# Kernel tuning notes

Measured on AMD Instinct MI355X. Metric: run time of the kernel, lower is better.

Reference implementation:

```python
import jax, jax.numpy as jnp
import numpy as np

L, H, P_LOC = 32768, 512, 256  # seq len, in/out dim, local state dim (conj_sym: P//2)
DT_MIN, DT_MAX = 1e-3, 1e-1
STEP_RESCALE = 1.0


def setup_inputs() -> dict:
    key = jax.random.key(0)
    ks = jax.random.split(key, 10)
    # stable eigenvalues: negative real part (mimics HiPPO init real part -1/2)
    Lambda_re = -0.1 - jax.random.uniform(ks[0], (P_LOC,), dtype=jnp.float32)
    Lambda_im = jax.random.normal(ks[1], (P_LOC,), dtype=jnp.float32) * jnp.pi
    B_re = jax.random.normal(ks[2], (P_LOC, H), dtype=jnp.float32) / jnp.sqrt(2.0 * H)
    B_im = jax.random.normal(ks[3], (P_LOC, H), dtype=jnp.float32) / jnp.sqrt(2.0 * H)
    C_re = jax.random.normal(ks[4], (H, P_LOC), dtype=jnp.float32) / jnp.sqrt(2.0 * P_LOC)
    C_im = jax.random.normal(ks[5], (H, P_LOC), dtype=jnp.float32) / jnp.sqrt(2.0 * P_LOC)
    D = jax.random.normal(ks[6], (H,), dtype=jnp.float32)
    u01 = jax.random.uniform(ks[7], (P_LOC,), dtype=jnp.float32)
    log_step = u01 * (jnp.log(DT_MAX) - jnp.log(DT_MIN)) + jnp.log(DT_MIN)
    input_sequence = jax.random.normal(ks[8], (L, H), dtype=jnp.float32)
    integration_timesteps = jax.random.uniform(ks[9], (L,), dtype=jnp.float32)
    return {
        "input_sequence": input_sequence,
        "integration_timesteps": integration_timesteps,
        "Lambda_re": Lambda_re, "Lambda_im": Lambda_im,
        "B_re": B_re, "B_im": B_im,
        "C_re": C_re, "C_im": C_im,
        "D": D, "log_step": log_step,
    }


def _binop(q_i, q_j):
    A_i, b_i = q_i
    A_j, b_j = q_j
    return (A_j * A_i, A_j * b_i + b_j)


def reference(input_sequence, integration_timesteps, Lambda_re, Lambda_im,
              B_re, B_im, C_re, C_im, D, log_step):
    Lambda = Lambda_re + 1j * Lambda_im          # (P,)
    B = B_re + 1j * B_im                         # (P, H)
    C_tilde = C_re + 1j * C_im                   # (H, P)
    step = STEP_RESCALE * jnp.exp(log_step)      # (P,)
    # ZOH discretization per timestep: Delta[l,p] = step[p] * dt[l]
    Delta = integration_timesteps[:, None] * step[None, :]          # (L, P)
    Lambda_bar = jnp.exp(Lambda[None, :] * Delta)                   # (L, P) complex
    gamma_bar = (Lambda_bar - 1.0) / Lambda[None, :]                # (L, P) complex
    Bu = gamma_bar * jnp.einsum("lh,ph->lp", input_sequence.astype(B.dtype), B)
    _, xs = jax.lax.associative_scan(_binop, (Lambda_bar, Bu))      # (L, P)
    # conj_sym=True -> output is 2 * Re(C x)
    ys = 2.0 * jnp.einsum("lp,hp->lh", xs, C_tilde).real            # (L, H)
    return ys + D[None, :] * input_sequence
```

## Files before the change

### kernel.cpp

```cpp
#include <hip/hip_runtime.h>
#include <math.h>

#define L_SEQ 32768
#define H_DIM 512
#define P_DIM 256
#define K_DIM 512
#define CHUNK 32
#define NCHUNK (L_SEQ / CHUNK)

typedef __bf16 bf16x8 __attribute__((ext_vector_type(8)));
typedef float floatx4 __attribute__((ext_vector_type(4)));

__device__ __forceinline__ void gll16(const void* g, void* l) {
    __builtin_amdgcn_global_load_lds(
        (__attribute__((address_space(1))) void*)(g),
        (__attribute__((address_space(3))) void*)(l), 16, 0, 0);
}

__global__ __launch_bounds__(512) void build_kernel(
    const float* __restrict__ Bre, const float* __restrict__ Bim,
    const float* __restrict__ Cre, const float* __restrict__ Cim,
    __bf16* __restrict__ B2, __bf16* __restrict__ C2)
{
    const int b = blockIdx.x;
    const int t = threadIdx.x;
    if (b < 256) {
        B2[(2 * b) * 512 + t]     = (__bf16)Bre[b * H_DIM + t];
        B2[(2 * b + 1) * 512 + t] = (__bf16)Bim[b * H_DIM + t];
    } else {
        const int h = b - 256;
        const int p = t & 255;
        if (t < 256)
            C2[h * 512 + 2 * p]     = (__bf16)Cre[h * P_DIM + p];
        else
            C2[h * 512 + 2 * p + 1] = (__bf16)(-Cim[h * P_DIM + p]);
    }
}

__global__ __launch_bounds__(256) void gemm1_kernel(
    const float* __restrict__ A,
    const __bf16* __restrict__ Bm,
    __bf16* __restrict__ Out)
{
    __shared__ float  Asf[128 * 32];
    __shared__ __bf16 Bs [128 * 32];

    const int tid = threadIdx.x;
    const int w  = tid >> 6;
    const int ln = tid & 63;
    const int bm = blockIdx.x;
    const int bn = blockIdx.y;

    floatx4 acc[4][4];
    #pragma unroll
    for (int i = 0; i < 4; ++i)
        #pragma unroll
        for (int j = 0; j < 4; ++j)
            acc[i][j] = (floatx4){0.f, 0.f, 0.f, 0.f};

    const int a_r = ln >> 3;
    const int a_c = (ln & 7) << 2;
    const int b_r = ln >> 2;
    const int b_c = (ln & 3) << 3;
    const size_t brow = (size_t)(bn * 128 + w * 16 + b_r) * K_DIM;

    float*  lA[4];
    size_t  gAr[4];
    #pragma unroll
    for (int q = 0; q < 4; ++q) {
        lA[q] = Asf + (q * 32 + w * 8) * 32;
        gAr[q] = (size_t)(bm * 128 + q * 32 + w * 8 + a_r) * K_DIM;
    }
    __bf16* lB0 = Bs + w * 512;
    __bf16* lB1 = Bs + 2048 + w * 512;

    const int wm = (w >> 1) * 64;
    const int wn = (w & 1) * 64;
    const int fr = ln & 15;
    const int fq = (ln >> 4) * 8;

    for (int kt = 0; kt < K_DIM; kt += 32) {
        __syncthreads();
        #pragma unroll
        for (int q = 0; q < 4; ++q)
            gll16(A + gAr[q] + kt + a_c, lA[q]);
        gll16(Bm + brow + kt + b_c,                      lB0);
        gll16(Bm + brow + (size_t)64 * K_DIM + kt + b_c, lB1);
        __syncthreads();

        bf16x8 a[4], b[4];
        #pragma unroll
        for (int mt = 0; mt < 4; ++mt) {
            floatx4 a0 = *(floatx4*)&Asf[(wm + mt * 16 + fr) * 32 + fq];
            floatx4 a1 = *(floatx4*)&Asf[(wm + mt * 16 + fr) * 32 + fq + 4];
            #pragma unroll
            for (int r = 0; r < 4; ++r) {
                a[mt][r]     = (__bf16)a0[r];
                a[mt][4 + r] = (__bf16)a1[r];
            }
        }
        #pragma unroll
        for (int nt = 0; nt < 4; ++nt)
            b[nt] = *(bf16x8*)&Bs[(wn + nt * 16 + fr) * 32 + fq];

        #pragma unroll
        for (int mt = 0; mt < 4; ++mt)
            #pragma unroll
            for (int nt = 0; nt < 4; ++nt)
                acc[mt][nt] = __builtin_amdgcn_mfma_f32_16x16x32_bf16(
                    a[mt], b[nt], acc[mt][nt], 0, 0, 0);
    }

    const int rq = (ln >> 4) * 4;
    #pragma unroll
    for (int mt = 0; mt < 4; ++mt) {
        const int gro = bm * 128 + wm + mt * 16 + rq;
        #pragma unroll
        for (int nt = 0; nt < 4; ++nt) {
            const int gco = bn * 128 + wn + nt * 16 + (ln & 15);
            #pragma unroll
            for (int r = 0; r < 4; ++r)
                Out[(size_t)(gro + r) * 512 + gco] = (__bf16)acc[mt][nt][r];
        }
    }
}

__global__ __launch_bounds__(256) void gemm2_kernel(
    const __bf16* __restrict__ A,
    const __bf16* __restrict__ Bm,
    float* __restrict__ Out,
    const float* __restrict__ U,
    const float* __restrict__ Dv)
{
    __shared__ __bf16 As[128 * 32];
    __shared__ __bf16 Bs[128 * 32];

    const int tid = threadIdx.x;
    const int w  = tid >> 6;
    const int ln = tid & 63;
    const int bm = blockIdx.x;
    const int bn = blockIdx.y;

    floatx4 acc[4][4];
    #pragma unroll
    for (int i = 0; i < 4; ++i)
        #pragma unroll
        for (int j = 0; j < 4; ++j)
            acc[i][j] = (floatx4){0.f, 0.f, 0.f, 0.f};

    const int lr = ln >> 2;
    const int lce = (ln & 3) << 3;
    const size_t arow = (size_t)(bm * 128 + w * 16 + lr) * K_DIM;
    const size_t brow = (size_t)(bn * 128 + w * 16 + lr) * K_DIM;

    __bf16* lA0 = As + w * 512;
    __bf16* lA1 = As + 2048 + w * 512;
    __bf16* lB0 = Bs + w * 512;
    __bf16* lB1 = Bs + 2048 + w * 512;

    const int wm = (w >> 1) * 64;
    const int wn = (w & 1) * 64;
    const int fr = ln & 15;
    const int fq = (ln >> 4) * 8;

    for (int kt = 0; kt < K_DIM; kt += 32) {
        __syncthreads();
        gll16(A  + arow + kt + lce,                      lA0);
        gll16(A  + arow + (size_t)64 * K_DIM + kt + lce, lA1);
        gll16(Bm + brow + kt + lce,                      lB0);
        gll16(Bm + brow + (size_t)64 * K_DIM + kt + lce, lB1);
        __syncthreads();

        bf16x8 a[4], b[4];
        #pragma unroll
        for (int mt = 0; mt < 4; ++mt)
            a[mt] = *(bf16x8*)&As[(wm + mt * 16 + fr) * 32 + fq];
        #pragma unroll
        for (int nt = 0; nt < 4; ++nt)
            b[nt] = *(bf16x8*)&Bs[(wn + nt * 16 + fr) * 32 + fq];

        #pragma unroll
        for (int mt = 0; mt < 4; ++mt)
            #pragma unroll
            for (int nt = 0; nt < 4; ++nt)
                acc[mt][nt] = __builtin_amdgcn_mfma_f32_16x16x32_bf16(
                    a[mt], b[nt], acc[mt][nt], 0, 0, 0);
    }

    const int rq = (ln >> 4) * 4;
    #pragma unroll
    for (int mt = 0; mt < 4; ++mt) {
        const int gro = bm * 128 + wm + mt * 16 + rq;
        #pragma unroll
        for (int nt = 0; nt < 4; ++nt) {
            const int gco = bn * 128 + wn + nt * 16 + (ln & 15);
            const float dh = Dv[gco];
            #pragma unroll
            for (int r = 0; r < 4; ++r) {
                const size_t o = (size_t)(gro + r) * 512 + gco;
                Out[o] = 2.0f * acc[mt][nt][r] + dh * U[o];
            }
        }
    }
}

template <int WRITE_X>
__global__ __launch_bounds__(256) void scan_chunk_kernel(
    const float* __restrict__ dts,
    const float* __restrict__ Lre_g, const float* __restrict__ Lim_g,
    const float* __restrict__ logstep,
    unsigned int* __restrict__ G2u,
    float4* __restrict__ Agg,
    const float2* __restrict__ Carry)
{
    const int p = threadIdx.x;
    const int c = blockIdx.x;
    const int base = c * CHUNK;

    unsigned int g[CHUNK];
    float dt[CHUNK];
    #pragma unroll
    for (int i = 0; i < CHUNK; ++i)
        g[i] = G2u[(size_t)(base + i) * 256 + p];
    #pragma unroll
    for (int i = 0; i < CHUNK; ++i)
        dt[i] = dts[base + i];

    const float lre = Lre_g[p];
    const float lim = Lim_g[p];
    const float stp = __expf(logstep[p]);
    const float inv_den = 1.0f / (lre * lre + lim * lim);

    float Are = 1.0f, Aim = 0.0f;
    float xre, xim;
    if (WRITE_X) {
        float2 cc = Carry[c * P_DIM + p];
        xre = cc.x; xim = cc.y;
    } else {
        xre = 0.0f; xim = 0.0f;
    }

    #pragma unroll
    for (int i = 0; i < CHUNK; ++i) {
        const float d = stp * dt[i];
        const float er = __expf(lre * d);
        const float sn = __sinf(lim * d);
        const float cs = __cosf(lim * d);
        const float are = er * cs;
        const float aim = er * sn;
        const float am1 = are - 1.0f;
        const float gr = (am1 * lre + aim * lim) * inv_den;
        const float gi = (aim * lre - am1 * lim) * inv_den;

        const float ure = __uint_as_float(g[i] << 16);
        const float uim = __uint_as_float(g[i] & 0xffff0000u);
        const float bre = gr * ure - gi * uim;
        const float bim = gr * uim + gi * ure;

        const float nxre = are * xre - aim * xim + bre;
        const float nxim = are * xim + aim * xre + bim;
        xre = nxre; xim = nxim;

        if (WRITE_X) {
            __bf16 xr = (__bf16)xre;
            __bf16 xi = (__bf16)xim;
            unsigned int o = (unsigned int)*(unsigned short*)&xr |
                             ((unsigned int)*(unsigned short*)&xi << 16);
            G2u[(size_t)(base + i) * 256 + p] = o;
        } else {
            const float nAre = are * Are - aim * Aim;
            const float nAim = are * Aim + aim * Are;
            Are = nAre; Aim = nAim;
        }
    }

    if (!WRITE_X)
        Agg[p * NCHUNK + c] = make_float4(Are, Aim, xre, xim);
}

struct CT { float Ar, Ai, br, bi; };

__device__ __forceinline__ CT ct_compose(const CT& f, const CT& s) {
    CT r;
    r.Ar = s.Ar * f.Ar - s.Ai * f.Ai;
    r.Ai = s.Ar * f.Ai + s.Ai * f.Ar;
    r.br = s.Ar * f.br - s.Ai * f.bi + s.br;
    r.bi = s.Ar * f.bi + s.Ai * f.br + s.bi;
    return r;
}

__global__ __launch_bounds__(256) void carry_shfl_kernel(
    const float4* __restrict__ Agg,
    float2* __restrict__ Carry)
{
    const int pch = blockIdx.x;
    const int t  = threadIdx.x;
    const int ln = t & 63;
    const int wv = t >> 6;

    __shared__ float4 wtot[4];

    CT v[4];
    #pragma unroll
    for (int i = 0; i < 4; ++i) {
        float4 f = Agg[(size_t)pch * NCHUNK + 4 * t + i];
        v[i].Ar = f.x; v[i].Ai = f.y; v[i].br = f.z; v[i].bi = f.w;
    }
    CT val = v[0];
    #pragma unroll
    for (int i = 1; i < 4; ++i) val = ct_compose(val, v[i]);

    #pragma unroll
    for (int off = 1; off < 64; off <<= 1) {
        CT o;
        o.Ar = __shfl_up(val.Ar, off);
        o.Ai = __shfl_up(val.Ai, off);
        o.br = __shfl_up(val.br, off);
        o.bi = __shfl_up(val.bi, off);
        if (ln >= off) val = ct_compose(o, val);
    }

    CT lexcl;
    lexcl.Ar = __shfl_up(val.Ar, 1);
    lexcl.Ai = __shfl_up(val.Ai, 1);
    lexcl.br = __shfl_up(val.br, 1);
    lexcl.bi = __shfl_up(val.bi, 1);
    if (ln == 0) { lexcl.Ar = 1.f; lexcl.Ai = 0.f; lexcl.br = 0.f; lexcl.bi = 0.f; }

    if (ln == 63) wtot[wv] = make_float4(val.Ar, val.Ai, val.br, val.bi);
    __syncthreads();

    CT wpre; wpre.Ar = 1.f; wpre.Ai = 0.f; wpre.br = 0.f; wpre.bi = 0.f;
    for (int i = 0; i < wv; ++i) {
        float4 f = wtot[i];
        CT tt; tt.Ar = f.x; tt.Ai = f.y; tt.br = f.z; tt.bi = f.w;
        wpre = ct_compose(wpre, tt);
    }

    CT E = ct_compose(wpre, lexcl);
    #pragma unroll
    for (int i = 0; i < 4; ++i) {
        Carry[(size_t)(4 * t + i) * P_DIM + pch] = make_float2(E.br, E.bi);
        E = ct_compose(E, v[i]);
    }
}

extern "C" void kernel_launch(void* const* d_in, const int* in_sizes, int n_in,
                              void* d_out, int out_size, void* d_ws, size_t ws_size,
                              hipStream_t stream) {
    const float* U       = (const float*)d_in[0];
    const float* dts     = (const float*)d_in[1];
    const float* Lre     = (const float*)d_in[2];
    const float* Lim     = (const float*)d_in[3];
    const float* Bre     = (const float*)d_in[4];
    const float* Bim     = (const float*)d_in[5];
    const float* Cre     = (const float*)d_in[6];
    const float* Cim     = (const float*)d_in[7];
    const float* Dv      = (const float*)d_in[8];
    const float* logstep = (const float*)d_in[9];
    float* out = (float*)d_out;

    char* ws = (char*)d_ws;
    __bf16* G2 = (__bf16*)ws;
    __bf16* B2 = (__bf16*)(ws + (size_t)L_SEQ * 512 * 2);
    __bf16* C2 = B2 + 512 * 512;
    float4* Agg = (float4*)(C2 + 512 * 512);
    float2* Carry = (float2*)(Agg + (size_t)P_DIM * NCHUNK);

    build_kernel<<<768, 512, 0, stream>>>(Bre, Bim, Cre, Cim, B2, C2);

    dim3 g1(L_SEQ / 128, 4);
    gemm1_kernel<<<g1, 256, 0, stream>>>(U, B2, G2);

    unsigned int* G2u = (unsigned int*)G2;
    scan_chunk_kernel<0><<<NCHUNK, 256, 0, stream>>>(
        dts, Lre, Lim, logstep, G2u, Agg, nullptr);
    carry_shfl_kernel<<<P_DIM, 256, 0, stream>>>(Agg, Carry);
    scan_chunk_kernel<1><<<NCHUNK, 256, 0, stream>>>(
        dts, Lre, Lim, logstep, G2u, nullptr, Carry);

    dim3 g2(L_SEQ / 128, 4);
    gemm2_kernel<<<g2, 256, 0, stream>>>(G2, C2, out, U, Dv);
}
```

Measured before the change: 227.3 us.

## Fuse ZOH discretization into GEMM1 epilogue and store fp16 decay factors

Moves the per-timestep exp/sin/cos discretization and gamma multiplication into the GEMM1 epilogue. The epilogue writes Bu in bf16 plus Lambda_bar in fp16 to a new workspace buffer. Both scan passes then only load precomputed coefficients, so the transcendentals are evaluated once instead of twice. In exchange it adds an extra 32 MB write and two extra reads of the A buffer, and lowers the decay factor to fp16 precision. The fused path is only taken when the workspace is large enough.

```diff
diff --git a/kernel.cpp b/kernel.cpp
--- a/kernel.cpp
+++ b/kernel.cpp
@@ -37,10 +37,15 @@
     }
 }
 
+template <int FUSED>
 __global__ __launch_bounds__(256) void gemm1_kernel(
     const float* __restrict__ A,
     const __bf16* __restrict__ Bm,
-    __bf16* __restrict__ Out)
+    __bf16* __restrict__ Outb,
+    unsigned short* __restrict__ Outa,
+    const float* __restrict__ dts,
+    const float* __restrict__ Lre_g, const float* __restrict__ Lim_g,
+    const float* __restrict__ logstep)
 {
     __shared__ float  Asf[128 * 32];
     __shared__ __bf16 Bs [128 * 32];
@@ -118,9 +123,39 @@
         #pragma unroll
         for (int nt = 0; nt < 4; ++nt) {
             const int gco = bn * 128 + wn + nt * 16 + (ln & 15);
-            #pragma unroll
-            for (int r = 0; r < 4; ++r)
-                Out[(size_t)(gro + r) * 512 + gco] = (__bf16)acc[mt][nt][r];
+            if (FUSED) {
+                const int p    = gco >> 1;
+                const int isim = gco & 1;
+                const float lre = Lre_g[p];
+                const float lim = Lim_g[p];
+                const float stp = __expf(logstep[p]);
+                const float inv_den = 1.0f / (lre * lre + lim * lim);
+                #pragma unroll
+                for (int r = 0; r < 4; ++r) {
+                    const int l = gro + r;
+                    const float d  = stp * dts[l];
+                    const float er = __expf(lre * d);
+                    const float sn = __sinf(lim * d);
+                    const float cs = __cosf(lim * d);
+                    const float are = er * cs;
+                    const float aim = er * sn;
+                    const float am1 = are - 1.0f;
+                    const float gr = (am1 * lre + aim * lim) * inv_den;
+                    const float gi = (aim * lre - am1 * lim) * inv_den;
+                    const float v  = acc[mt][nt][r];
+                    const float pv = __shfl_xor(v, 1);
+                    const float bout = isim ? (gr * v + gi * pv)
+                                            : (gr * v - gi * pv);
+                    const float aout = isim ? aim : are;
+                    Outb[(size_t)l * 512 + gco] = (__bf16)bout;
+                    const _Float16 ah = (_Float16)aout;
+                    Outa[(size_t)l * 512 + gco] = *(const unsigned short*)&ah;
+                }
+            } else {
+                #pragma unroll
+                for (int r = 0; r < 4; ++r)
+                    Outb[(size_t)(gro + r) * 512 + gco] = (__bf16)acc[mt][nt][r];
+            }
         }
     }
 }
@@ -205,11 +240,9 @@
 }
 
 template <int WRITE_X>
-__global__ __launch_bounds__(256) void scan_chunk_kernel(
-    const float* __restrict__ dts,
-    const float* __restrict__ Lre_g, const float* __restrict__ Lim_g,
-    const float* __restrict__ logstep,
+__global__ __launch_bounds__(256) void scan_affine_kernel(
     unsigned int* __restrict__ G2u,
+    const unsigned int* __restrict__ A2u,
     float4* __restrict__ Agg,
     const float2* __restrict__ Carry)
 {
@@ -217,19 +250,13 @@
     const int c = blockIdx.x;
     const int base = c * CHUNK;
 
-    unsigned int g[CHUNK];
-    float dt[CHUNK];
+    unsigned int gb[CHUNK], ga[CHUNK];
     #pragma unroll
     for (int i = 0; i < CHUNK; ++i)
-        g[i] = G2u[(size_t)(base + i) * 256 + p];
+        gb[i] = G2u[(size_t)(base + i) * 256 + p];
     #pragma unroll
     for (int i = 0; i < CHUNK; ++i)
-        dt[i] = dts[base + i];
-
-    const float lre = Lre_g[p];
-    const float lim = Lim_g[p];
-    const float stp = __expf(logstep[p]);
-    const float inv_den = 1.0f / (lre * lre + lim * lim);
+        ga[i] = A2u[(size_t)(base + i) * 256 + p];
 
     float Are = 1.0f, Aim = 0.0f;
     float xre, xim;
@@ -242,20 +269,12 @@
 
     #pragma unroll
     for (int i = 0; i < CHUNK; ++i) {
-        const float d = stp * dt[i];
-        const float er = __expf(lre * d);
-        const float sn = __sinf(lim * d);
-        const float cs = __cosf(lim * d);
-        const float are = er * cs;
-        const float aim = er * sn;
-        const float am1 = are - 1.0f;
-        const float gr = (am1 * lre + aim * lim) * inv_den;
-        const float gi = (aim * lre - am1 * lim) * inv_den;
-
-        const float ure = __uint_as_float(g[i] << 16);
-        const float uim = __uint_as_float(g[i] & 0xffff0000u);
-        const float bre = gr * ure - gi * uim;
-        const float bim = gr * uim + gi * ure;
+        const float bre = __uint_as_float(gb[i] << 16);
+        const float bim = __uint_as_float(gb[i] & 0xffff0000u);
+        unsigned short alo = (unsigned short)(ga[i] & 0xffffu);
+        unsigned short ahi = (unsigned short)(ga[i] >> 16);
+        const float are = (float)*(const _Float16*)&alo;
+        const float aim = (float)*(const _Float16*)&ahi;
 
         const float nxre = are * xre - aim * xim + bre;
         const float nxim = are * xim + aim * xre + bim;
@@ -275,7 +294,81 @@
     }
 
     if (!WRITE_X)
-        Agg[p * NCHUNK + c] = make_float4(Are, Aim, xre, xim);
+        Agg[(size_t)p * NCHUNK + c] = make_float4(Are, Aim, xre, xim);
+}
+
+template <int WRITE_X>
+__global__ __launch_bounds__(256) void scan_chunk_kernel(
+    const float* __restrict__ dts,
+    const float* __restrict__ Lre_g, const float* __restrict__ Lim_g,
+    const float* __restrict__ logstep,
+    unsigned int* __restrict__ G2u,
+    float4* __restrict__ Agg,
+    const float2* __restrict__ Carry)
+{
+    const int p = threadIdx.x;
+    const int c = blockIdx.x;
+    const int base = c * CHUNK;
+
+    unsigned int g[CHUNK];
+    float dt[CHUNK];
+    #pragma unroll
+    for (int i = 0; i < CHUNK; ++i)
+        g[i] = G2u[(size_t)(base + i) * 256 + p];
+    #pragma unroll
+    for (int i = 0; i < CHUNK; ++i)
+        dt[i] = dts[base + i];
+
+    const float lre = Lre_g[p];
+    const float lim = Lim_g[p];
+    const float stp = __expf(logstep[p]);
+    const float inv_den = 1.0f / (lre * lre + lim * lim);
+
+    float Are = 1.0f, Aim = 0.0f;
+    float xre, xim;
+    if (WRITE_X) {
+        float2 cc = Carry[c * P_DIM + p];
+        xre = cc.x; xim = cc.y;
+    } else {
+        xre = 0.0f; xim = 0.0f;
+    }
+
+    #pragma unroll
+    for (int i = 0; i < CHUNK; ++i) {
+        const float d = stp * dt[i];
+        const float er = __expf(lre * d);
+        const float sn = __sinf(lim * d);
+        const float cs = __cosf(lim * d);
+        const float are = er * cs;
+        const float aim = er * sn;
+        const float am1 = are - 1.0f;
+        const float gr = (am1 * lre + aim * lim) * inv_den;
+        const float gi = (aim * lre - am1 * lim) * inv_den;
+
+        const float ure = __uint_as_float(g[i] << 16);
+        const float uim = __uint_as_float(g[i] & 0xffff0000u);
+        const float bre = gr * ure - gi * uim;
+        const float bim = gr * uim + gi * ure;
+
+        const float nxre = are * xre - aim * xim + bre;
+        const float nxim = are * xim + aim * xre + bim;
+        xre = nxre; xim = nxim;
+
+        if (WRITE_X) {
+            __bf16 xr = (__bf16)xre;
+            __bf16 xi = (__bf16)xim;
+            unsigned int o = (unsigned int)*(unsigned short*)&xr |
+                             ((unsigned int)*(unsigned short*)&xi << 16);
+            G2u[(size_t)(base + i) * 256 + p] = o;
+        } else {
+            const float nAre = are * Are - aim * Aim;
+            const float nAim = are * Aim + aim * Are;
+            Are = nAre; Aim = nAim;
+        }
+    }
+
+    if (!WRITE_X)
+        Agg[(size_t)p * NCHUNK + c] = make_float4(Are, Aim, xre, xim);
 }
 
 struct CT { float Ar, Ai, br, bi; };
@@ -366,18 +459,37 @@
     __bf16* C2 = B2 + 512 * 512;
     float4* Agg = (float4*)(C2 + 512 * 512);
     float2* Carry = (float2*)(Agg + (size_t)P_DIM * NCHUNK);
+    unsigned short* A2 = (unsigned short*)(Carry + (size_t)NCHUNK * P_DIM);
+
+    const size_t base_need = (size_t)L_SEQ * 512 * 2 + 2 * 512 * 512 * 2
+                           + (size_t)P_DIM * NCHUNK * 16
+                           + (size_t)NCHUNK * P_DIM * 8;
+    const size_t fused_need = base_need + (size_t)L_SEQ * 512 * 2;
+    const bool fused = (ws_size >= fused_need);
 
     build_kernel<<<768, 512, 0, stream>>>(Bre, Bim, Cre, Cim, B2, C2);
 
     dim3 g1(L_SEQ / 128, 4);
-    gemm1_kernel<<<g1, 256, 0, stream>>>(U, B2, G2);
-
     unsigned int* G2u = (unsigned int*)G2;
-    scan_chunk_kernel<0><<<NCHUNK, 256, 0, stream>>>(
-        dts, Lre, Lim, logstep, G2u, Agg, nullptr);
-    carry_shfl_kernel<<<P_DIM, 256, 0, stream>>>(Agg, Carry);
-    scan_chunk_kernel<1><<<NCHUNK, 256, 0, stream>>>(
-        dts, Lre, Lim, logstep, G2u, nullptr, Carry);
+    const unsigned int* A2u = (const unsigned int*)A2;
+
+    if (fused) {
+        gemm1_kernel<1><<<g1, 256, 0, stream>>>(
+            U, B2, G2, A2, dts, Lre, Lim, logstep);
+        scan_affine_kernel<0><<<NCHUNK, 256, 0, stream>>>(
+            G2u, A2u, Agg, nullptr);
+        carry_shfl_kernel<<<P_DIM, 256, 0, stream>>>(Agg, Carry);
+        scan_affine_kernel<1><<<NCHUNK, 256, 0, stream>>>(
+            G2u, A2u, nullptr, Carry);
+    } else {
+        gemm1_kernel<0><<<g1, 256, 0, stream>>>(
+            U, B2, G2, nullptr, dts, Lre, Lim, logstep);
+        scan_chunk_kernel<0><<<NCHUNK, 256, 0, stream>>>(
+            dts, Lre, Lim, logstep, G2u, Agg, nullptr);
+        carry_shfl_kernel<<<P_DIM, 256, 0, stream>>>(Agg, Carry);
+        scan_chunk_kernel<1><<<NCHUNK, 256, 0, stream>>>(
+            dts, Lre, Lim, logstep, G2u, nullptr, Carry);
+    }
 
     dim3 g2(L_SEQ / 128, 4);
     gemm2_kernel<<<g2, 256, 0, stream>>>(G2, C2, out, U, Dv);
```

New measurement: 248.8 us. +9.4%, slower.
